# Optimization experiments

Measured on AMD Instinct MI355X. Metric: run time of the kernel, lower is better.

The kernel has to match this reference:

```python
import jax, jax.numpy as jnp
import numpy as np

N = 50000   # nodes
E = 800000  # edges (avg degree 16)
IN = 384    # input gene features
H = 256     # hidden
EPS = 1e-12 # F.normalize eps


def setup_inputs() -> dict:
    key = jax.random.key(0)
    ks = jax.random.split(key, 10)
    x = jax.random.uniform(ks[0], (N, IN), dtype=jnp.float32) * 10.0  # count-like
    src = jax.random.randint(ks[1], (E,), 0, N, dtype=jnp.int32)
    dst = jax.random.randint(ks[2], (E,), 0, N, dtype=jnp.int32)
    def lin(k, din):
        return (jax.random.normal(k, (din, H), dtype=jnp.float32) / np.sqrt(din).astype(np.float32))
    return {
        'x': x, 'src': src, 'dst': dst,
        'W_self0': lin(ks[3], IN), 'W_neigh0': lin(ks[4], IN), 'b0': jnp.zeros((H,), jnp.float32),
        'W_self1': lin(ks[5], H), 'W_neigh1': lin(ks[6], H), 'b1': jnp.zeros((H,), jnp.float32),
        'W_self2': lin(ks[7], H), 'W_neigh2': lin(ks[8], H), 'b2': jnp.zeros((H,), jnp.float32),
    }


def _sage_mean(h, src, dst, Ws, Wn, b):
    # gather neighbor feats along edges, mean-aggregate into dst nodes
    msg = h[src]                                             # [E, d]
    agg = jax.ops.segment_sum(msg, dst, num_segments=N)      # [N, d]
    deg = jax.ops.segment_sum(jnp.ones((E,), h.dtype), dst, num_segments=N)
    h_neigh = agg / jnp.maximum(deg, 1.0)[:, None]           # isolated nodes -> 0
    return h @ Ws + h_neigh @ Wn + b


def _l2norm(h):
    n = jnp.sqrt(jnp.sum(h * h, axis=-1, keepdims=True))
    return h / jnp.maximum(n, EPS)


def reference(x, src, dst, W_self0, W_neigh0, b0, W_self1, W_neigh1, b1, W_self2, W_neigh2, b2):
    h = jnp.log1p(x)
    # layers 0..n-2: SAGEConv -> relu -> L2 normalize
    h = _l2norm(jax.nn.relu(_sage_mean(h, src, dst, W_self0, W_neigh0, b0)))
    h = _l2norm(jax.nn.relu(_sage_mean(h, src, dst, W_self1, W_neigh1, b1)))
    # last layer: plain SAGEConv (feat_drop inactive in eval)
    h = _sage_mean(h, src, dst, W_self2, W_neigh2, b2)
    return h
```

## Files before the change

kernel.cpp:

```cpp
#include <hip/hip_runtime.h>
#include <hip/hip_bf16.h>

#define N_NODES 50000
#define N_EDGES 800000
#define DIM_IN  384
#define DIM_H   256

typedef __bf16 bf16x8 __attribute__((ext_vector_type(8)));
typedef float  f32x4  __attribute__((ext_vector_type(4)));

static __device__ __forceinline__ ushort f2bf(float f) {
  uint u = __float_as_uint(f);
  u += 0x7fffu + ((u >> 16) & 1u);
  return (ushort)(u >> 16);
}
static __device__ __forceinline__ float bf_lo(uint u) { return __uint_as_float(u << 16); }
static __device__ __forceinline__ float bf_hi(uint u) { return __uint_as_float(u & 0xffff0000u); }

typedef const __attribute__((address_space(1))) void* gas_p;
typedef __attribute__((address_space(3))) void* las_p;
static __device__ __forceinline__ void gload16(const void* g, void* l) {
  __builtin_amdgcn_global_load_lds((gas_p)g, (las_p)l, 16, 0, 0);
}

static __device__ __forceinline__ float log1p_fast(float x) {
  return __logf(1.0f + x);
}

#define L1_BLOCKS ((N_NODES * DIM_IN / 4 + 255) / 256)
#define HIST_BLOCKS ((N_EDGES + 255) / 256)

__global__ void log1p_hist_kernel(const float* __restrict__ x, ushort* __restrict__ h,
                                  const int* __restrict__ dst, int* __restrict__ deg) {
  int bid = blockIdx.x;
  if (bid < L1_BLOCKS) {
    int i = bid * 256 + threadIdx.x;
    if (i >= N_NODES * DIM_IN / 4) return;
    float4 v = reinterpret_cast<const float4*>(x)[i];
    ushort4 o;
    o.x = f2bf(log1p_fast(v.x));
    o.y = f2bf(log1p_fast(v.y));
    o.z = f2bf(log1p_fast(v.z));
    o.w = f2bf(log1p_fast(v.w));
    reinterpret_cast<ushort4*>(h)[i] = o;
  } else {
    int i = (bid - L1_BLOCKS) * 256 + threadIdx.x;
    if (i < N_EDGES) atomicAdd(&deg[dst[i]], 1);
  }
}

__global__ void scan1_kernel(const int* __restrict__ deg, int* __restrict__ tmp,
                             int* __restrict__ bsum) {
  __shared__ int buf[256];
  int t = threadIdx.x, i = blockIdx.x * 256 + t;
  int v = (i < N_NODES) ? deg[i] : 0;
  buf[t] = v;
  __syncthreads();
  int x = v;
#pragma unroll
  for (int off = 1; off < 256; off <<= 1) {
    int y = (t >= off) ? buf[t - off] : 0;
    __syncthreads();
    x += y;
    buf[t] = x;
    __syncthreads();
  }
  if (i < N_NODES) tmp[i] = x - v;
  if (t == 255) bsum[blockIdx.x] = x;
}

__global__ void scan2_kernel(int* __restrict__ bsum, int nb) {
  __shared__ int buf[256];
  int t = threadIdx.x;
  int v = (t < nb) ? bsum[t] : 0;
  buf[t] = v;
  __syncthreads();
  int x = v;
#pragma unroll
  for (int off = 1; off < 256; off <<= 1) {
    int y = (t >= off) ? buf[t - off] : 0;
    __syncthreads();
    x += y;
    buf[t] = x;
    __syncthreads();
  }
  if (t < nb) bsum[t] = x - v;
}

__global__ void scan3_kernel(const int* __restrict__ tmp, const int* __restrict__ bsum,
                             int* __restrict__ rowptr, int* __restrict__ cursor) {
  int i = blockIdx.x * 256 + threadIdx.x;
  if (i >= N_NODES) return;
  int r = tmp[i] + bsum[i >> 8];
  rowptr[i] = r;
  cursor[i] = r;
}

static __device__ __forceinline__ int permc(int p) {
  return ((p >> 7) << 7) + ((p & 7) << 4) + ((p >> 3) & 15);
}
static __device__ __forceinline__ void pack_one(const float* W, ushort* out, int local, bool perm) {
  int k = local >> 8, col = local & 255;
  int kc = k >> 5, kgd = (k >> 3) & 3, e = k & 7;
  int kgs = kgd ^ ((col >> 1) & 3);
  int krow = perm ? permc(k) : k;
  out[((size_t)kc * 256 + col) * 32 + kgs * 8 + e] = f2bf(W[krow * 256 + col]);
}

#define FILL_BLOCKS ((N_EDGES + 255) / 256)
#define PACK_TOT (2 * DIM_IN * 256 + 4 * DIM_H * 256)
#define PACK_BLOCKS ((PACK_TOT + 255) / 256)

__global__ void fill_pack_kernel(const int* __restrict__ src, const int* __restrict__ dst,
                                 int* __restrict__ cursor, ushort* __restrict__ csr,
                                 const float* W0s, const float* W0n, const float* W1s,
                                 const float* W1n, const float* W2s, const float* W2n,
                                 ushort* o0s, ushort* o0n, ushort* o1s, ushort* o1n,
                                 ushort* o2s, ushort* o2n) {
  int bid = blockIdx.x;
  if (bid < FILL_BLOCKS) {
    int i = bid * 256 + threadIdx.x;
    if (i >= N_EDGES) return;
    int d = dst[i];
    int p = atomicAdd(&cursor[d], 1);
    csr[p] = (ushort)src[i];
  } else {
    int idx = (bid - FILL_BLOCKS) * 256 + threadIdx.x;
    const int SZ0 = DIM_IN * 256;
    const int SZ1 = DIM_H * 256;
    if (idx < SZ0) pack_one(W0s, o0s, idx, false);
    else if (idx < 2 * SZ0) pack_one(W0n, o0n, idx - SZ0, false);
    else {
      int j = idx - 2 * SZ0;
      int w = j / SZ1, local = j - w * SZ1;
      if (w == 0) pack_one(W1s, o1s, local, true);
      else if (w == 1) pack_one(W1n, o1n, local, true);
      else if (w == 2) pack_one(W2s, o2s, local, true);
      else if (w == 3) pack_one(W2n, o2n, local, true);
    }
  }
}

template <int K, bool SF32>
__global__ __launch_bounds__(256, 2) void gemm_dual_kernel(const ushort* __restrict__ A,
                                                           const ushort* __restrict__ Bs,
                                                           const ushort* __restrict__ Bn,
                                                           const float* __restrict__ bias,
                                                           void* __restrict__ Sout,
                                                           unsigned char* __restrict__ Yq,
                                                           float* __restrict__ scales) {
  constexpr int KC = K / 32;
  constexpr int NT = 2 * KC;
  __shared__ ushort Al[2][4096];
  __shared__ ushort Bl[2][8192];
  __shared__ float red[2][2][4][4][4];

  const int tid = threadIdx.x;
  const int wv = tid >> 6, lane = tid & 63, lj = lane & 15, lg = lane >> 4;
  const int wm = wv >> 1, wn = wv & 1;
  const int r0 = blockIdx.x * 128;

  int grow[2], akgd[2];
#pragma unroll
  for (int j = 0; j < 2; ++j) {
    int d = tid + j * 256;
    int row = d >> 2, kgs = d & 3;
    akgd[j] = kgs ^ ((row >> 1) & 3);
    int r = r0 + row;
    grow[j] = r < N_NODES ? r : N_NODES - 1;
  }

  int aoff[4], boff[8];
#pragma unroll
  for (int mf = 0; mf < 4; ++mf) {
    int row = wm * 64 + mf * 16 + lj;
    aoff[mf] = row * 32 + (lg ^ ((row >> 1) & 3)) * 8;
  }
#pragma unroll
  for (int f = 0; f < 8; ++f) {
    int col = wn * 128 + f * 16 + lj;
    boff[f] = col * 32 + (lg ^ ((col >> 1) & 3)) * 8;
  }

  auto stage = [&](int t, int bb) {
    int p = t >= KC;
    int kc = t - p * KC;
    const ushort* Bp = p ? Bn : Bs;
#pragma unroll
    for (int j = 0; j < 2; ++j)
      gload16(A + (size_t)grow[j] * K + kc * 32 + akgd[j] * 8,
              (char*)&Al[bb][0] + j * 4096 + wv * 1024);
#pragma unroll
    for (int j = 0; j < 4; ++j)
      gload16(Bp + (size_t)kc * 8192 + (tid + j * 256) * 8,
              (char*)&Bl[bb][0] + j * 4096 + wv * 1024);
  };

  float bvv[8];
#pragma unroll
  for (int f = 0; f < 8; ++f) bvv[f] = bias[wn * 128 + f * 16 + lj];

  f32x4 acc[4][8];
#pragma unroll
  for (int mf = 0; mf < 4; ++mf)
#pragma unroll
    for (int f = 0; f < 8; ++f) acc[mf][f] = (f32x4){0.f, 0.f, 0.f, 0.f};

  stage(0, 0);
  __syncthreads();
  int b = 0;
  for (int t = 0; t < NT; ++t) {
    if (t + 1 < NT) stage(t + 1, b ^ 1);
    bf16x8 av[4], bv[8];
#pragma unroll
    for (int mf = 0; mf < 4; ++mf)
      av[mf] = *reinterpret_cast<const bf16x8*>(&Al[b][aoff[mf]]);
#pragma unroll
    for (int f = 0; f < 8; ++f)
      bv[f] = *reinterpret_cast<const bf16x8*>(&Bl[b][boff[f]]);
#pragma unroll
    for (int mf = 0; mf < 4; ++mf)
#pragma unroll
      for (int f = 0; f < 8; ++f)
        acc[mf][f] = __builtin_amdgcn_mfma_f32_16x16x32_bf16(av[mf], bv[f], acc[mf][f], 0, 0, 0);
    if (t == KC - 1) {
#pragma unroll
      for (int mf = 0; mf < 4; ++mf)
#pragma unroll
        for (int e = 0; e < 4; ++e) {
          int row = r0 + wm * 64 + mf * 16 + lg * 4 + e;
          if (row < N_NODES) {
            if constexpr (SF32) {
              float* pS = (float*)Sout + (size_t)row * 256 + wn * 128 + lj * 8;
              float4 v0 = {acc[mf][0][e] + bvv[0], acc[mf][1][e] + bvv[1],
                           acc[mf][2][e] + bvv[2], acc[mf][3][e] + bvv[3]};
              float4 v1 = {acc[mf][4][e] + bvv[4], acc[mf][5][e] + bvv[5],
                           acc[mf][6][e] + bvv[6], acc[mf][7][e] + bvv[7]};
              *reinterpret_cast<float4*>(pS) = v0;
              *reinterpret_cast<float4*>(pS + 4) = v1;
            } else {
              ushort* pS = (ushort*)Sout + (size_t)row * 256 + wn * 128 + lj * 8;
              uint4 o;
              o.x = (uint)f2bf(acc[mf][0][e] + bvv[0]) | ((uint)f2bf(acc[mf][1][e] + bvv[1]) << 16);
              o.y = (uint)f2bf(acc[mf][2][e] + bvv[2]) | ((uint)f2bf(acc[mf][3][e] + bvv[3]) << 16);
              o.z = (uint)f2bf(acc[mf][4][e] + bvv[4]) | ((uint)f2bf(acc[mf][5][e] + bvv[5]) << 16);
              o.w = (uint)f2bf(acc[mf][6][e] + bvv[6]) | ((uint)f2bf(acc[mf][7][e] + bvv[7]) << 16);
              *reinterpret_cast<uint4*>(pS) = o;
            }
          }
        }
#pragma unroll
      for (int mf = 0; mf < 4; ++mf)
#pragma unroll
        for (int f = 0; f < 8; ++f) acc[mf][f] = (f32x4){0.f, 0.f, 0.f, 0.f};
    }
    __syncthreads();
    b ^= 1;
  }

  float rmax[4][4];
#pragma unroll
  for (int mf = 0; mf < 4; ++mf)
#pragma unroll
    for (int e = 0; e < 4; ++e) {
      float m = 0.f;
#pragma unroll
      for (int f = 0; f < 8; ++f) m = fmaxf(m, fabsf(acc[mf][f][e]));
      rmax[mf][e] = m;
    }
#pragma unroll
  for (int mf = 0; mf < 4; ++mf)
#pragma unroll
    for (int e = 0; e < 4; ++e) {
      float m = rmax[mf][e];
      m = fmaxf(m, __shfl_xor(m, 1));
      m = fmaxf(m, __shfl_xor(m, 2));
      m = fmaxf(m, __shfl_xor(m, 4));
      m = fmaxf(m, __shfl_xor(m, 8));
      rmax[mf][e] = m;
    }
  if (lj == 0) {
#pragma unroll
    for (int mf = 0; mf < 4; ++mf)
#pragma unroll
      for (int e = 0; e < 4; ++e) red[wn][wm][mf][lg][e] = rmax[mf][e];
  }
  __syncthreads();
#pragma unroll
  for (int mf = 0; mf < 4; ++mf)
#pragma unroll
    for (int e = 0; e < 4; ++e) {
      float m = fmaxf(fmaxf(red[0][wm][mf][lg][e], red[1][wm][mf][lg][e]), 1e-30f);
      float inv_s = 127.0f / m;
      int row = r0 + wm * 64 + mf * 16 + lg * 4 + e;
      if (row < N_NODES) {
        uint lo = 0, hi = 0;
#pragma unroll
        for (int f = 0; f < 4; ++f) {
          int q = (int)rintf(acc[mf][f][e] * inv_s) + 128;
          q = max(0, min(255, q));
          lo |= (uint)q << (8 * f);
        }
#pragma unroll
        for (int f = 4; f < 8; ++f) {
          int q = (int)rintf(acc[mf][f][e] * inv_s) + 128;
          q = max(0, min(255, q));
          hi |= (uint)q << (8 * (f - 4));
        }
        *reinterpret_cast<uint2*>(Yq + (size_t)row * 256 + wn * 128 + lj * 8) = make_uint2(lo, hi);
        if (wn == 0 && lj == 0) scales[row] = m * (1.0f / 127.0f);
      }
    }
}

template <bool FINAL>
__global__ __launch_bounds__(256) void gather_kernel(const unsigned char* __restrict__ Yq,
                                                     const float* __restrict__ scales,
                                                     const void* __restrict__ Sin,
                                                     const int* __restrict__ rowptr,
                                                     const int* __restrict__ deg,
                                                     const ushort* __restrict__ csr,
                                                     void* __restrict__ outv) {
  int node = blockIdx.x * 8 + (threadIdx.x >> 5);
  if (node >= N_NODES) return;
  int hl = threadIdx.x & 31;
  int start = rowptr[node];
  int d = deg[node];
  float acc[8];
#pragma unroll
  for (int i = 0; i < 8; ++i) acc[i] = 0.0f;
  float stot = 0.f;

  auto ub = [](uint u, int j) { return (float)((u >> (8 * j)) & 0xffu); };
  int e = 0;
  for (; e + 4 <= d; e += 4) {
    int s0 = csr[start + e], s1 = csr[start + e + 1];
    int s2 = csr[start + e + 2], s3 = csr[start + e + 3];
    float c0 = scales[s0], c1 = scales[s1], c2 = scales[s2], c3 = scales[s3];
    uint2 q0 = *reinterpret_cast<const uint2*>(Yq + (size_t)s0 * 256 + hl * 8);
    uint2 q1 = *reinterpret_cast<const uint2*>(Yq + (size_t)s1 * 256 + hl * 8);
    uint2 q2 = *reinterpret_cast<const uint2*>(Yq + (size_t)s2 * 256 + hl * 8);
    uint2 q3 = *reinterpret_cast<const uint2*>(Yq + (size_t)s3 * 256 + hl * 8);
    stot += c0 + c1 + c2 + c3;
#pragma unroll
    for (int j = 0; j < 4; ++j) {
      acc[j]     += c0 * ub(q0.x, j) + c1 * ub(q1.x, j) + c2 * ub(q2.x, j) + c3 * ub(q3.x, j);
      acc[4 + j] += c0 * ub(q0.y, j) + c1 * ub(q1.y, j) + c2 * ub(q2.y, j) + c3 * ub(q3.y, j);
    }
  }
  for (; e < d; ++e) {
    int s = csr[start + e];
    float c = scales[s];
    uint2 q = *reinterpret_cast<const uint2*>(Yq + (size_t)s * 256 + hl * 8);
    stot += c;
#pragma unroll
    for (int j = 0; j < 4; ++j) {
      acc[j]     += c * ub(q.x, j);
      acc[4 + j] += c * ub(q.y, j);
    }
  }

  float invd = 1.0f / fmaxf((float)d, 1.0f);
  float nb[8];
#pragma unroll
  for (int j = 0; j < 8; ++j) nb[j] = (acc[j] - 128.0f * stot) * invd;

  if constexpr (FINAL) {
    const float* S = (const float*)Sin + (size_t)node * 256 + hl * 8;
    float4 s0 = *reinterpret_cast<const float4*>(S);
    float4 s1 = *reinterpret_cast<const float4*>(S + 4);
    float sv[8] = {s0.x, s0.y, s0.z, s0.w, s1.x, s1.y, s1.z, s1.w};
    float* out = (float*)outv + (size_t)node * 256 + (hl >> 4) * 128 + (hl & 15);
#pragma unroll
    for (int f = 0; f < 8; ++f) out[f * 16] = nb[f] + sv[f];
  } else {
    const ushort* S = (const ushort*)Sin + (size_t)node * 256 + hl * 8;
    uint4 sv = *reinterpret_cast<const uint4*>(S);
    uint su[4] = {sv.x, sv.y, sv.z, sv.w};
    float v[8];
    float ssq = 0.f;
#pragma unroll
    for (int i = 0; i < 4; ++i) {
      float a = fmaxf(nb[2 * i] + bf_lo(su[i]), 0.0f);
      float b = fmaxf(nb[2 * i + 1] + bf_hi(su[i]), 0.0f);
      v[2 * i] = a; v[2 * i + 1] = b;
      ssq += a * a + b * b;
    }
    ssq += __shfl_xor(ssq, 1);
    ssq += __shfl_xor(ssq, 2);
    ssq += __shfl_xor(ssq, 4);
    ssq += __shfl_xor(ssq, 8);
    ssq += __shfl_xor(ssq, 16);
    float rn = 1.0f / fmaxf(sqrtf(ssq), 1e-12f);
    uint o[4];
#pragma unroll
    for (int i = 0; i < 4; ++i) {
      uint lo = f2bf(v[2 * i] * rn);
      uint hi = f2bf(v[2 * i + 1] * rn);
      o[i] = lo | (hi << 16);
    }
    *reinterpret_cast<uint4*>((ushort*)outv + (size_t)node * 256 + hl * 8) =
        make_uint4(o[0], o[1], o[2], o[3]);
  }
}

extern "C" void kernel_launch(void* const* d_in, const int* in_sizes, int n_in,
                              void* d_out, int out_size, void* d_ws, size_t ws_size,
                              hipStream_t stream) {
  const float* x   = (const float*)d_in[0];
  const int*   src = (const int*)d_in[1];
  const int*   dst = (const int*)d_in[2];
  const float* Ws0 = (const float*)d_in[3];
  const float* Wn0 = (const float*)d_in[4];
  const float* b0  = (const float*)d_in[5];
  const float* Ws1 = (const float*)d_in[6];
  const float* Wn1 = (const float*)d_in[7];
  const float* b1  = (const float*)d_in[8];
  const float* Ws2 = (const float*)d_in[9];
  const float* Wn2 = (const float*)d_in[10];
  const float* b2  = (const float*)d_in[11];

  uintptr_t p = ((uintptr_t)d_ws + 255) & ~(uintptr_t)255;
  auto carve = [&](size_t bytes) {
    void* r = (void*)p;
    p += (bytes + 255) & ~(size_t)255;
    return r;
  };
  ushort* h0 = (ushort*)carve((size_t)N_NODES * DIM_IN * 2);
  ushort* h2 = h0;
  ushort* S_mid = (ushort*)carve((size_t)N_NODES * DIM_H * 2 * 2);
  ushort* h1 = S_mid + (size_t)N_NODES * DIM_H;
  float*  S2f = (float*)S_mid;
  unsigned char* Yq = (unsigned char*)carve((size_t)N_NODES * 256);
  float* scales = (float*)carve((size_t)N_NODES * 4);
  ushort* Ws0p = (ushort*)carve((size_t)DIM_IN * 256 * 2);
  ushort* Wn0p = (ushort*)carve((size_t)DIM_IN * 256 * 2);
  ushort* Ws1p = (ushort*)carve((size_t)DIM_H * 256 * 2);
  ushort* Wn1p = (ushort*)carve((size_t)DIM_H * 256 * 2);
  ushort* Ws2p = (ushort*)carve((size_t)DIM_H * 256 * 2);
  ushort* Wn2p = (ushort*)carve((size_t)DIM_H * 256 * 2);
  int* deg    = (int*)carve((size_t)N_NODES * 4);
  int* rowptr = (int*)carve((size_t)N_NODES * 4);
  int* cursor = (int*)carve((size_t)N_NODES * 4);
  int* stmp   = (int*)carve((size_t)N_NODES * 4);
  int* bsum   = (int*)carve(256 * 4);
  ushort* csr = (ushort*)carve((size_t)N_EDGES * 2);

  hipMemsetAsync(deg, 0, (size_t)N_NODES * 4, stream);

  log1p_hist_kernel<<<L1_BLOCKS + HIST_BLOCKS, 256, 0, stream>>>(x, h0, dst, deg);

  const int scanBlocks = (N_NODES + 255) / 256;
  scan1_kernel<<<scanBlocks, 256, 0, stream>>>(deg, stmp, bsum);
  scan2_kernel<<<1, 256, 0, stream>>>(bsum, scanBlocks);
  scan3_kernel<<<scanBlocks, 256, 0, stream>>>(stmp, bsum, rowptr, cursor);

  fill_pack_kernel<<<FILL_BLOCKS + PACK_BLOCKS, 256, 0, stream>>>(
      src, dst, cursor, csr, Ws0, Wn0, Ws1, Wn1, Ws2, Wn2,
      Ws0p, Wn0p, Ws1p, Wn1p, Ws2p, Wn2p);

  const int gatherBlocks = (N_NODES + 7) / 8;
  const int gemmBlocks   = (N_NODES + 127) / 128;

  gemm_dual_kernel<DIM_IN, false><<<gemmBlocks, 256, 0, stream>>>(h0, Ws0p, Wn0p, b0, S_mid, Yq, scales);
  gather_kernel<false><<<gatherBlocks, 256, 0, stream>>>(Yq, scales, S_mid, rowptr, deg, csr, h1);
  gemm_dual_kernel<DIM_H, false><<<gemmBlocks, 256, 0, stream>>>(h1, Ws1p, Wn1p, b1, S_mid, Yq, scales);
  gather_kernel<false><<<gatherBlocks, 256, 0, stream>>>(Yq, scales, S_mid, rowptr, deg, csr, h2);
  gemm_dual_kernel<DIM_H, true><<<gemmBlocks, 256, 0, stream>>>(h2, Ws2p, Wn2p, b2, S2f, Yq, scales);
  gather_kernel<true><<<gatherBlocks, 256, 0, stream>>>(Yq, scales, S2f, rowptr, deg, csr, d_out);
}
```

Before: 330.7 us.

## Fuse weight packing into prep and CSR fill into layer-0 GEMM, interleave blocks

Weight packing moves into the log1p/histogram prep kernel, and those blocks are interleaved one degree block per six log1p blocks. The CSR fill now runs inside the first GEMM kernel, with eight fill blocks interleaved per GEMM block. This removes one launch and lets latency-bound atomic work overlap with compute and bandwidth work. The last layer's self term is also stored as bf16 instead of fp32, which saves traffic but adds rounding error to the final output.

```diff
diff --git a/kernel.cpp b/kernel.cpp
--- a/kernel.cpp
+++ b/kernel.cpp
@@ -27,25 +27,59 @@
   return __logf(1.0f + x);
 }
 
-#define L1_BLOCKS ((N_NODES * DIM_IN / 4 + 255) / 256)
-#define HIST_BLOCKS ((N_EDGES + 255) / 256)
-
-__global__ void log1p_hist_kernel(const float* __restrict__ x, ushort* __restrict__ h,
-                                  const int* __restrict__ dst, int* __restrict__ deg) {
+static __device__ __forceinline__ int permc(int p) {
+  return ((p >> 7) << 7) + ((p & 7) << 4) + ((p >> 3) & 15);
+}
+static __device__ __forceinline__ void pack_one(const float* W, ushort* out, int local, bool perm) {
+  int k = local >> 8, col = local & 255;
+  int kc = k >> 5, kgd = (k >> 3) & 3, e = k & 7;
+  int kgs = kgd ^ ((col >> 1) & 3);
+  int krow = perm ? permc(k) : k;
+  out[((size_t)kc * 256 + col) * 32 + kgs * 8 + e] = f2bf(W[krow * 256 + col]);
+}
+
+#define HIST_BLOCKS 3125
+#define L1_BLOCKS   18750
+#define STRIPE1_TOT (HIST_BLOCKS * 7)
+#define PACK_TOT (2 * DIM_IN * 256 + 4 * DIM_H * 256)
+#define PACK_BLOCKS ((PACK_TOT + 255) / 256)
+
+__global__ void prep_kernel(const float* __restrict__ x, ushort* __restrict__ h,
+                            const int* __restrict__ dst, int* __restrict__ deg,
+                            const float* W0s, const float* W0n, const float* W1s,
+                            const float* W1n, const float* W2s, const float* W2n,
+                            ushort* o0s, ushort* o0n, ushort* o1s, ushort* o1n,
+                            ushort* o2s, ushort* o2n) {
   int bid = blockIdx.x;
-  if (bid < L1_BLOCKS) {
-    int i = bid * 256 + threadIdx.x;
-    if (i >= N_NODES * DIM_IN / 4) return;
-    float4 v = reinterpret_cast<const float4*>(x)[i];
-    ushort4 o;
-    o.x = f2bf(log1p_fast(v.x));
-    o.y = f2bf(log1p_fast(v.y));
-    o.z = f2bf(log1p_fast(v.z));
-    o.w = f2bf(log1p_fast(v.w));
-    reinterpret_cast<ushort4*>(h)[i] = o;
+  if (bid < STRIPE1_TOT) {
+    int g = bid / 7, r = bid - g * 7;
+    if (r == 0) {
+      int i = g * 256 + threadIdx.x;
+      if (i < N_EDGES) atomicAdd(&deg[dst[i]], 1);
+    } else {
+      int i = (g * 6 + (r - 1)) * 256 + threadIdx.x;
+      float4 v = reinterpret_cast<const float4*>(x)[i];
+      ushort4 o;
+      o.x = f2bf(log1p_fast(v.x));
+      o.y = f2bf(log1p_fast(v.y));
+      o.z = f2bf(log1p_fast(v.z));
+      o.w = f2bf(log1p_fast(v.w));
+      reinterpret_cast<ushort4*>(h)[i] = o;
+    }
   } else {
-    int i = (bid - L1_BLOCKS) * 256 + threadIdx.x;
-    if (i < N_EDGES) atomicAdd(&deg[dst[i]], 1);
+    int idx = (bid - STRIPE1_TOT) * 256 + threadIdx.x;
+    const int SZ0 = DIM_IN * 256;
+    const int SZ1 = DIM_H * 256;
+    if (idx < SZ0) pack_one(W0s, o0s, idx, false);
+    else if (idx < 2 * SZ0) pack_one(W0n, o0n, idx - SZ0, false);
+    else if (idx < PACK_TOT) {
+      int j = idx - 2 * SZ0;
+      int w = j / SZ1, local = j - w * SZ1;
+      if (w == 0) pack_one(W1s, o1s, local, true);
+      else if (w == 1) pack_one(W1n, o1n, local, true);
+      else if (w == 2) pack_one(W2s, o2s, local, true);
+      else pack_one(W2n, o2n, local, true);
+    }
   }
 }
 
@@ -96,69 +130,21 @@
   cursor[i] = r;
 }
 
-static __device__ __forceinline__ int permc(int p) {
-  return ((p >> 7) << 7) + ((p & 7) << 4) + ((p >> 3) & 15);
-}
-static __device__ __forceinline__ void pack_one(const float* W, ushort* out, int local, bool perm) {
-  int k = local >> 8, col = local & 255;
-  int kc = k >> 5, kgd = (k >> 3) & 3, e = k & 7;
-  int kgs = kgd ^ ((col >> 1) & 3);
-  int krow = perm ? permc(k) : k;
-  out[((size_t)kc * 256 + col) * 32 + kgs * 8 + e] = f2bf(W[krow * 256 + col]);
-}
-
-#define FILL_BLOCKS ((N_EDGES + 255) / 256)
-#define PACK_TOT (2 * DIM_IN * 256 + 4 * DIM_H * 256)
-#define PACK_BLOCKS ((PACK_TOT + 255) / 256)
-
-__global__ void fill_pack_kernel(const int* __restrict__ src, const int* __restrict__ dst,
-                                 int* __restrict__ cursor, ushort* __restrict__ csr,
-                                 const float* W0s, const float* W0n, const float* W1s,
-                                 const float* W1n, const float* W2s, const float* W2n,
-                                 ushort* o0s, ushort* o0n, ushort* o1s, ushort* o1n,
-                                 ushort* o2s, ushort* o2n) {
-  int bid = blockIdx.x;
-  if (bid < FILL_BLOCKS) {
-    int i = bid * 256 + threadIdx.x;
-    if (i >= N_EDGES) return;
-    int d = dst[i];
-    int p = atomicAdd(&cursor[d], 1);
-    csr[p] = (ushort)src[i];
-  } else {
-    int idx = (bid - FILL_BLOCKS) * 256 + threadIdx.x;
-    const int SZ0 = DIM_IN * 256;
-    const int SZ1 = DIM_H * 256;
-    if (idx < SZ0) pack_one(W0s, o0s, idx, false);
-    else if (idx < 2 * SZ0) pack_one(W0n, o0n, idx - SZ0, false);
-    else {
-      int j = idx - 2 * SZ0;
-      int w = j / SZ1, local = j - w * SZ1;
-      if (w == 0) pack_one(W1s, o1s, local, true);
-      else if (w == 1) pack_one(W1n, o1n, local, true);
-      else if (w == 2) pack_one(W2s, o2s, local, true);
-      else if (w == 3) pack_one(W2n, o2n, local, true);
-    }
-  }
-}
-
-template <int K, bool SF32>
-__global__ __launch_bounds__(256, 2) void gemm_dual_kernel(const ushort* __restrict__ A,
-                                                           const ushort* __restrict__ Bs,
-                                                           const ushort* __restrict__ Bn,
-                                                           const float* __restrict__ bias,
-                                                           void* __restrict__ Sout,
-                                                           unsigned char* __restrict__ Yq,
-                                                           float* __restrict__ scales) {
+template <int K>
+static __device__ void gemm_dual_body(int blk, ushort* Al, ushort* Bl, float* red,
+                                      const ushort* __restrict__ A,
+                                      const ushort* __restrict__ Bs,
+                                      const ushort* __restrict__ Bn,
+                                      const float* __restrict__ bias,
+                                      ushort* __restrict__ Sout,
+                                      unsigned char* __restrict__ Yq,
+                                      float* __restrict__ scales) {
   constexpr int KC = K / 32;
   constexpr int NT = 2 * KC;
-  __shared__ ushort Al[2][4096];
-  __shared__ ushort Bl[2][8192];
-  __shared__ float red[2][2][4][4][4];
-
   const int tid = threadIdx.x;
   const int wv = tid >> 6, lane = tid & 63, lj = lane & 15, lg = lane >> 4;
   const int wm = wv >> 1, wn = wv & 1;
-  const int r0 = blockIdx.x * 128;
+  const int r0 = blk * 128;
 
   int grow[2], akgd[2];
 #pragma unroll
@@ -189,11 +175,11 @@
 #pragma unroll
     for (int j = 0; j < 2; ++j)
       gload16(A + (size_t)grow[j] * K + kc * 32 + akgd[j] * 8,
-              (char*)&Al[bb][0] + j * 4096 + wv * 1024);
+              (char*)(Al + bb * 4096) + j * 4096 + wv * 1024);
 #pragma unroll
     for (int j = 0; j < 4; ++j)
       gload16(Bp + (size_t)kc * 8192 + (tid + j * 256) * 8,
-              (char*)&Bl[bb][0] + j * 4096 + wv * 1024);
+              (char*)(Bl + bb * 8192) + j * 4096 + wv * 1024);
   };
 
   float bvv[8];
@@ -214,10 +200,10 @@
     bf16x8 av[4], bv[8];
 #pragma unroll
     for (int mf = 0; mf < 4; ++mf)
-      av[mf] = *reinterpret_cast<const bf16x8*>(&Al[b][aoff[mf]]);
+      av[mf] = *reinterpret_cast<const bf16x8*>(Al + b * 4096 + aoff[mf]);
 #pragma unroll
     for (int f = 0; f < 8; ++f)
-      bv[f] = *reinterpret_cast<const bf16x8*>(&Bl[b][boff[f]]);
+      bv[f] = *reinterpret_cast<const bf16x8*>(Bl + b * 8192 + boff[f]);
 #pragma unroll
     for (int mf = 0; mf < 4; ++mf)
 #pragma unroll
@@ -230,23 +216,13 @@
         for (int e = 0; e < 4; ++e) {
           int row = r0 + wm * 64 + mf * 16 + lg * 4 + e;
           if (row < N_NODES) {
-            if constexpr (SF32) {
-              float* pS = (float*)Sout + (size_t)row * 256 + wn * 128 + lj * 8;
-              float4 v0 = {acc[mf][0][e] + bvv[0], acc[mf][1][e] + bvv[1],
-                           acc[mf][2][e] + bvv[2], acc[mf][3][e] + bvv[3]};
-              float4 v1 = {acc[mf][4][e] + bvv[4], acc[mf][5][e] + bvv[5],
-                           acc[mf][6][e] + bvv[6], acc[mf][7][e] + bvv[7]};
-              *reinterpret_cast<float4*>(pS) = v0;
-              *reinterpret_cast<float4*>(pS + 4) = v1;
-            } else {
-              ushort* pS = (ushort*)Sout + (size_t)row * 256 + wn * 128 + lj * 8;
-              uint4 o;
-              o.x = (uint)f2bf(acc[mf][0][e] + bvv[0]) | ((uint)f2bf(acc[mf][1][e] + bvv[1]) << 16);
-              o.y = (uint)f2bf(acc[mf][2][e] + bvv[2]) | ((uint)f2bf(acc[mf][3][e] + bvv[3]) << 16);
-              o.z = (uint)f2bf(acc[mf][4][e] + bvv[4]) | ((uint)f2bf(acc[mf][5][e] + bvv[5]) << 16);
-              o.w = (uint)f2bf(acc[mf][6][e] + bvv[6]) | ((uint)f2bf(acc[mf][7][e] + bvv[7]) << 16);
-              *reinterpret_cast<uint4*>(pS) = o;
-            }
+            ushort* pS = Sout + (size_t)row * 256 + wn * 128 + lj * 8;
+            uint4 o;
+            o.x = (uint)f2bf(acc[mf][0][e] + bvv[0]) | ((uint)f2bf(acc[mf][1][e] + bvv[1]) << 16);
+            o.y = (uint)f2bf(acc[mf][2][e] + bvv[2]) | ((uint)f2bf(acc[mf][3][e] + bvv[3]) << 16);
+            o.z = (uint)f2bf(acc[mf][4][e] + bvv[4]) | ((uint)f2bf(acc[mf][5][e] + bvv[5]) << 16);
+            o.w = (uint)f2bf(acc[mf][6][e] + bvv[6]) | ((uint)f2bf(acc[mf][7][e] + bvv[7]) << 16);
+            *reinterpret_cast<uint4*>(pS) = o;
           }
         }
 #pragma unroll
@@ -266,13 +242,6 @@
       float m = 0.f;
 #pragma unroll
       for (int f = 0; f < 8; ++f) m = fmaxf(m, fabsf(acc[mf][f][e]));
-      rmax[mf][e] = m;
-    }
-#pragma unroll
-  for (int mf = 0; mf < 4; ++mf)
-#pragma unroll
-    for (int e = 0; e < 4; ++e) {
-      float m = rmax[mf][e];
       m = fmaxf(m, __shfl_xor(m, 1));
       m = fmaxf(m, __shfl_xor(m, 2));
       m = fmaxf(m, __shfl_xor(m, 4));
@@ -283,14 +252,16 @@
 #pragma unroll
     for (int mf = 0; mf < 4; ++mf)
 #pragma unroll
-      for (int e = 0; e < 4; ++e) red[wn][wm][mf][lg][e] = rmax[mf][e];
+      for (int e = 0; e < 4; ++e)
+        red[(wn * 2 + wm) * 64 + mf * 16 + lg * 4 + e] = rmax[mf][e];
   }
   __syncthreads();
 #pragma unroll
   for (int mf = 0; mf < 4; ++mf)
 #pragma unroll
     for (int e = 0; e < 4; ++e) {
-      float m = fmaxf(fmaxf(red[0][wm][mf][lg][e], red[1][wm][mf][lg][e]), 1e-30f);
+      float m = fmaxf(fmaxf(red[(0 * 2 + wm) * 64 + mf * 16 + lg * 4 + e],
+                            red[(1 * 2 + wm) * 64 + mf * 16 + lg * 4 + e]), 1e-30f);
       float inv_s = 127.0f / m;
       int row = r0 + wm * 64 + mf * 16 + lg * 4 + e;
       if (row < N_NODES) {
@@ -313,10 +284,45 @@
     }
 }
 
+#define GEMM_BLOCKS ((N_NODES + 127) / 128)
+#define GF_TOT (GEMM_BLOCKS * 9)
+
+__global__ __launch_bounds__(256, 2) void gemm0_fill_kernel(
+    const ushort* __restrict__ A, const ushort* __restrict__ Bs,
+    const ushort* __restrict__ Bn, const float* __restrict__ bias,
+    ushort* __restrict__ Sout, unsigned char* __restrict__ Yq, float* __restrict__ scales,
+    const int* __restrict__ src, const int* __restrict__ dst,
+    int* __restrict__ cursor, ushort* __restrict__ csr) {
+  __shared__ ushort Al[2 * 4096];
+  __shared__ ushort Bl[2 * 8192];
+  __shared__ float red[256];
+  int g = blockIdx.x / 9, r = blockIdx.x - g * 9;
+  if (r == 0) {
+    gemm_dual_body<DIM_IN>(g, Al, Bl, red, A, Bs, Bn, bias, Sout, Yq, scales);
+  } else {
+    int i = (g * 8 + (r - 1)) * 256 + threadIdx.x;
+    if (i < N_EDGES) {
+      int d = dst[i];
+      int p = atomicAdd(&cursor[d], 1);
+      csr[p] = (ushort)src[i];
+    }
+  }
+}
+
+__global__ __launch_bounds__(256, 2) void gemm_dual_kernel(
+    const ushort* __restrict__ A, const ushort* __restrict__ Bs,
+    const ushort* __restrict__ Bn, const float* __restrict__ bias,
+    ushort* __restrict__ Sout, unsigned char* __restrict__ Yq, float* __restrict__ scales) {
+  __shared__ ushort Al[2 * 4096];
+  __shared__ ushort Bl[2 * 8192];
+  __shared__ float red[256];
+  gemm_dual_body<DIM_H>(blockIdx.x, Al, Bl, red, A, Bs, Bn, bias, Sout, Yq, scales);
+}
+
 template <bool FINAL>
 __global__ __launch_bounds__(256) void gather_kernel(const unsigned char* __restrict__ Yq,
                                                      const float* __restrict__ scales,
-                                                     const void* __restrict__ Sin,
+                                                     const ushort* __restrict__ Sin,
                                                      const int* __restrict__ rowptr,
                                                      const int* __restrict__ deg,
                                                      const ushort* __restrict__ csr,
@@ -365,18 +371,17 @@
 #pragma unroll
   for (int j = 0; j < 8; ++j) nb[j] = (acc[j] - 128.0f * stot) * invd;
 
+  uint4 sv = *reinterpret_cast<const uint4*>(Sin + (size_t)node * 256 + hl * 8);
+  uint su[4] = {sv.x, sv.y, sv.z, sv.w};
+
   if constexpr (FINAL) {
-    const float* S = (const float*)Sin + (size_t)node * 256 + hl * 8;
-    float4 s0 = *reinterpret_cast<const float4*>(S);
-    float4 s1 = *reinterpret_cast<const float4*>(S + 4);
-    float sv[8] = {s0.x, s0.y, s0.z, s0.w, s1.x, s1.y, s1.z, s1.w};
     float* out = (float*)outv + (size_t)node * 256 + (hl >> 4) * 128 + (hl & 15);
 #pragma unroll
-    for (int f = 0; f < 8; ++f) out[f * 16] = nb[f] + sv[f];
+    for (int i = 0; i < 4; ++i) {
+      out[(2 * i) * 16]     = nb[2 * i] + bf_lo(su[i]);
+      out[(2 * i + 1) * 16] = nb[2 * i + 1] + bf_hi(su[i]);
+    }
   } else {
-    const ushort* S = (const ushort*)Sin + (size_t)node * 256 + hl * 8;
-    uint4 sv = *reinterpret_cast<const uint4*>(S);
-    uint su[4] = {sv.x, sv.y, sv.z, sv.w};
     float v[8];
     float ssq = 0.f;
 #pragma unroll
@@ -428,9 +433,8 @@
   };
   ushort* h0 = (ushort*)carve((size_t)N_NODES * DIM_IN * 2);
   ushort* h2 = h0;
-  ushort* S_mid = (ushort*)carve((size_t)N_NODES * DIM_H * 2 * 2);
-  ushort* h1 = S_mid + (size_t)N_NODES * DIM_H;
-  float*  S2f = (float*)S_mid;
+  ushort* S_mid = (ushort*)carve((size_t)N_NODES * DIM_H * 2);
+  ushort* h1 = (ushort*)carve((size_t)N_NODES * DIM_H * 2);
   unsigned char* Yq = (unsigned char*)carve((size_t)N_NODES * 256);
   float* scales = (float*)carve((size_t)N_NODES * 4);
   ushort* Ws0p = (ushort*)carve((size_t)DIM_IN * 256 * 2);
@@ -448,24 +452,23 @@
 
   hipMemsetAsync(deg, 0, (size_t)N_NODES * 4, stream);
 
-  log1p_hist_kernel<<<L1_BLOCKS + HIST_BLOCKS, 256, 0, stream>>>(x, h0, dst, deg);
+  prep_kernel<<<STRIPE1_TOT + PACK_BLOCKS, 256, 0, stream>>>(
+      x, h0, dst, deg, Ws0, Wn0, Ws1, Wn1, Ws2, Wn2,
+      Ws0p, Wn0p, Ws1p, Wn1p, Ws2p, Wn2p);
 
   const int scanBlocks = (N_NODES + 255) / 256;
   scan1_kernel<<<scanBlocks, 256, 0, stream>>>(deg, stmp, bsum);
   scan2_kernel<<<1, 256, 0, stream>>>(bsum, scanBlocks);
   scan3_kernel<<<scanBlocks, 256, 0, stream>>>(stmp, bsum, rowptr, cursor);
 
-  fill_pack_kernel<<<FILL_BLOCKS + PACK_BLOCKS, 256, 0, stream>>>(
-      src, dst, cursor, csr, Ws0, Wn0, Ws1, Wn1, Ws2, Wn2,
-      Ws0p, Wn0p, Ws1p, Wn1p, Ws2p, Wn2p);
+  gemm0_fill_kernel<<<GF_TOT, 256, 0, stream>>>(h0, Ws0p, Wn0p, b0, S_mid, Yq, scales,
+                                                src, dst, cursor, csr);
 
   const int gatherBlocks = (N_NODES + 7) / 8;
-  const int gemmBlocks   = (N_NODES + 127) / 128;
-
-  gemm_dual_kernel<DIM_IN, false><<<gemmBlocks, 256, 0, stream>>>(h0, Ws0p, Wn0p, b0, S_mid, Yq, scales);
+
   gather_kernel<false><<<gatherBlocks, 256, 0, stream>>>(Yq, scales, S_mid, rowptr, deg, csr, h1);
-  gemm_dual_kernel<DIM_H, false><<<gemmBlocks, 256, 0, stream>>>(h1, Ws1p, Wn1p, b1, S_mid, Yq, scales);
+  gemm_dual_kernel<<<GEMM_BLOCKS, 256, 0, stream>>>(h1, Ws1p, Wn1p, b1, S_mid, Yq, scales);
   gather_kernel<false><<<gatherBlocks, 256, 0, stream>>>(Yq, scales, S_mid, rowptr, deg, csr, h2);
-  gemm_dual_kernel<DIM_H, true><<<gemmBlocks, 256, 0, stream>>>(h2, Ws2p, Wn2p, b2, S2f, Yq, scales);
-  gather_kernel<true><<<gatherBlocks, 256, 0, stream>>>(Yq, scales, S2f, rowptr, deg, csr, d_out);
-}
+  gemm_dual_kernel<<<GEMM_BLOCKS, 256, 0, stream>>>(h2, Ws2p, Wn2p, b2, S_mid, Yq, scales);
+  gather_kernel<true><<<gatherBlocks, 256, 0, stream>>>(Yq, scales, S_mid, rowptr, deg, csr, d_out);
+}
```

New measurement: 298.0 us. 9.9% less time.
